# Kernel optimization log

Hardware: AMD Instinct MI355X
Metric: run time of the kernel (lower is better)

## Reference

```python
import jax, jax.numpy as jnp
import numpy as np

K = 16
REP = 128
ASZ = 6
AENC = 64
BSK = 2048 * K  # bs*K flat batch


def _lin(k, fin, fout):
    return jax.random.normal(k, (fin, fout), jnp.float32) / np.float32(np.sqrt(fin))


def setup_inputs() -> dict:
    key = jax.random.key(0)
    ks = jax.random.split(key, 20)
    inp = {
        "lambda1": jax.random.normal(ks[0], (BSK, REP), jnp.float32),
        "actions": jax.random.normal(ks[1], (BSK, ASZ), jnp.float32),
    }
    # (fan_in, hidden, fan_out) per rlkit Mlp((hidden,), out, in)
    specs = {
        "le": (REP, REP, REP),            # lambda_encoder
        "ae": (ASZ, REP, AENC),           # action_encoder
        "aef": (AENC + REP, REP, REP),    # action_effect_network
        "aat": (AENC + REP, REP, 1),      # action_attention_network
        "pe": (2 * REP, 2 * REP, REP),    # pairwise_encoder_network
        "ie": (REP, REP, AENC),           # interaction_effect_network
        "ia": (REP, REP, 1),              # interaction_attention_network
        "fm": (AENC + REP, REP, REP),     # final_merge_network
    }
    i = 2
    for name, (fin, h, fout) in specs.items():
        inp[name + "_W1"] = _lin(ks[i], fin, h)
        inp[name + "_b1"] = jnp.zeros((h,), jnp.float32)
        inp[name + "_W2"] = _lin(ks[i + 1], h, fout)
        inp[name + "_b2"] = jnp.zeros((fout,), jnp.float32)
        i += 2
    return inp


def _mlp(x, W1, b1, W2, b2, out_act):
    h = jax.nn.elu(x @ W1 + b1)
    return out_act(h @ W2 + b2)


# constant all-pairs index lists (i != j), i-major as in the torch loop
_II = np.array([i for i in range(K) for j in range(K) if i != j])
_JJ = np.array([j for i in range(K) for j in range(K) if i != j])


def reference(lambda1, actions,
              le_W1, le_b1, le_W2, le_b2,
              ae_W1, ae_b1, ae_W2, ae_b2,
              aef_W1, aef_b1, aef_W2, aef_b2,
              aat_W1, aat_b1, aat_W2, aat_b2,
              pe_W1, pe_b1, pe_W2, pe_b2,
              ie_W1, ie_b1, ie_W2, ie_b2,
              ia_W1, ia_b1, ia_W2, ia_b2,
              fm_W1, fm_b1, fm_W2, fm_b2):
    elu, sig = jax.nn.elu, jax.nn.sigmoid
    ident = lambda z: z

    enc_flat = _mlp(lambda1, le_W1, le_b1, le_W2, le_b2, elu)        # (BSK, REP)
    a_enc = _mlp(actions, ae_W1, ae_b1, ae_W2, ae_b2, elu)           # (BSK, AENC)
    la = jnp.concatenate([enc_flat, a_enc], -1)                      # (BSK, REP+AENC)
    a_eff = _mlp(la, aef_W1, aef_b1, aef_W2, aef_b2, elu)            # (BSK, REP)
    a_att = _mlp(la, aat_W1, aat_b1, aat_W2, aat_b2, sig)            # (BSK, 1)
    enc = (a_eff * a_att).reshape(-1, K, REP)                        # (bs, K, REP)
    bs = enc.shape[0]

    # all ordered pairs (i, j), i != j -> concat sender/receiver states
    all_pairs = jnp.concatenate([enc[:, _II], enc[:, _JJ]], -1)      # (bs, K*(K-1), 2*REP)
    all_pairs = all_pairs.reshape(bs * K, K - 1, 2 * REP)

    pi = _mlp(all_pairs, pe_W1, pe_b1, pe_W2, pe_b2, elu)            # (bs*K, K-1, REP)
    effect = _mlp(pi, ie_W1, ie_b1, ie_W2, ie_b2, elu)               # (bs*K, K-1, AENC)
    attention = _mlp(pi, ia_W1, ia_b1, ia_W2, ia_b2, sig)            # (bs*K, K-1, 1)
    total_effect = (effect * attention).sum(1)                       # (bs*K, AENC)

    lam_eff = jnp.concatenate([enc_flat, total_effect], -1)          # (bs*K, REP+AENC)
    new_lambdas = _mlp(lam_eff, fm_W1, fm_b1, fm_W2, fm_b2, ident)   # (bs*K, REP)
    return new_lambdas
```

## Files before the change

### kernel.cpp

```cpp
#include <hip/hip_runtime.h>

typedef unsigned short ushort_t;
typedef unsigned int uint_t;
typedef short bf16x8 __attribute__((ext_vector_type(8)));
typedef float f32x4 __attribute__((ext_vector_type(4)));

#define MFMA16(a, b, c) __builtin_amdgcn_mfma_f32_16x16x32_bf16((a), (b), (c), 0, 0, 0)

__device__ __forceinline__ ushort_t f2bf(float f) {
  uint_t u = __float_as_uint(f);
  u += 0x7fffu + ((u >> 16) & 1u);
  return (ushort_t)(u >> 16);
}
__device__ __forceinline__ float bf2f(ushort_t h) {
  return __uint_as_float(((uint_t)h) << 16);
}
__device__ __forceinline__ float eluf(float x) {
  float e = __expf(x) - 1.0f;
  return x > 0.0f ? x : e;
}
__device__ __forceinline__ float sigmf(float x) {
  return 1.0f / (1.0f + __expf(-x));
}

constexpr int BSK = 32768;
constexpr size_t OFF_ENCF = 0;
constexpr size_t OFF_ENC  = 4194304;
constexpr size_t OFF_TEFF = 8388608;
constexpr size_t OFF_FR   = 10485760;

constexpr int FR_LE_W1  = 0;
constexpr int FR_LE_W2  = 16384;
constexpr int FR_AE_W2  = 32768;
constexpr int FR_AEF_W1 = 40960;
constexpr int FR_AAT_W1 = 65536;
constexpr int FR_AEF_W2 = 90112;
constexpr int FR_PE_W1  = 106496;
constexpr int FR_PE_W2  = 172032;
constexpr int FR_IE_W1  = 204800;
constexpr int FR_IE_W2  = 221184;
constexpr int FR_IA_W1  = 229376;
constexpr int FR_FM_W1  = 245760;
constexpr int FR_FM_W2  = 270336;

struct PrepDesc { const float* src; ushort_t* dst; int K; int N; };
struct PrepArgs { PrepDesc d[13]; };

__global__ __launch_bounds__(256) void prep_kernel(PrepArgs a) {
  PrepDesc p = a.d[blockIdx.y];
  int idx = blockIdx.x * 256 + threadIdx.x;
  if (idx >= p.K * p.N) return;
  int e = idx & 7;
  int lane = (idx >> 3) & 63;
  int f = idx >> 9;
  int ksteps = p.K >> 5;
  int kstep = f % ksteps;
  int ntile = f / ksteps;
  int k = kstep * 32 + ((lane >> 4) << 3) + e;
  int n = ntile * 16 + (lane & 15);
  p.dst[idx] = f2bf(p.src[k * p.N + n]);
}


template <int MT, int NT, int KS>
__device__ __forceinline__ void reg_gemm(const bf16x8 a[MT][KS],
                                         const ushort_t* __restrict__ wfrag,
                                         int ntile0, int lane, f32x4 acc[MT][NT]) {
  const f32x4 z = {0.f, 0.f, 0.f, 0.f};
#pragma unroll
  for (int nt = 0; nt < NT; ++nt) {
#pragma unroll
    for (int m = 0; m < MT; ++m) acc[m][nt] = z;
    const ushort_t* wf = wfrag + (size_t)((ntile0 + nt) * KS) * 512 + lane * 8;
#pragma unroll
    for (int ks = 0; ks < KS; ++ks) {
      bf16x8 bfr = *(const bf16x8*)(wf + ks * 512);
#pragma unroll
      for (int m = 0; m < MT; ++m) acc[m][nt] = MFMA16(a[m][ks], bfr, acc[m][nt]);
    }
  }
}

template <int MT, int NT, int KS>
__device__ __forceinline__ void lds_gemm(const ushort_t* __restrict__ Abase,
                                         const ushort_t* __restrict__ wfrag,
                                         int ntile0, int lane, f32x4 acc[MT][NT]) {
  const int r = lane & 15, q = lane >> 4;
  const int swz = (r & 7) << 4;
  bf16x8 a[MT][KS];
#pragma unroll
  for (int m = 0; m < MT; ++m)
#pragma unroll
    for (int ks = 0; ks < KS; ++ks) {
      int row = m * 16 + r;
      int colb = (ks * 64 + q * 16) ^ swz;
      a[m][ks] = *(const bf16x8*)((const char*)Abase + row * (KS * 64) + colb);
    }
  reg_gemm<MT, NT, KS>(a, wfrag, ntile0, lane, acc);
}

template <int MT, int NT, bool ELU>
__device__ __forceinline__ void add_bias_act(f32x4 acc[MT][NT], const float* __restrict__ bias,
                                             int col0, int lane) {
  const int r = lane & 15;
#pragma unroll
  for (int nt = 0; nt < NT; ++nt) {
    float bv = bias[col0 + nt * 16 + r];
#pragma unroll
    for (int m = 0; m < MT; ++m)
#pragma unroll
      for (int k = 0; k < 4; ++k) {
        float v = acc[m][nt][k] + bv;
        acc[m][nt][k] = ELU ? eluf(v) : v;
      }
  }
}

template <int MT, int NT, int CCB>
__device__ __forceinline__ void store_lds(ushort_t* Dbase, int col0, int lane,
                                          const f32x4 acc[MT][NT]) {
  const int cr = lane & 15, cq = lane >> 4;
#pragma unroll
  for (int m = 0; m < MT; ++m)
#pragma unroll
    for (int nt = 0; nt < NT; ++nt)
#pragma unroll
      for (int k = 0; k < 4; ++k) {
        int row = m * 16 + cq * 4 + k;
        int colb = ((col0 + nt * 16 + cr) * 2) ^ ((row & 7) << 4);
        *(ushort_t*)((char*)Dbase + row * CCB + colb) = f2bf(acc[m][nt][k]);
      }
}

template <int MT, int NT>
__device__ __forceinline__ void store_global(ushort_t* __restrict__ G, int row0, int ncols,
                                             int col0, int lane, const f32x4 acc[MT][NT]) {
  const int cr = lane & 15, cq = lane >> 4;
#pragma unroll
  for (int m = 0; m < MT; ++m)
#pragma unroll
    for (int nt = 0; nt < NT; ++nt)
#pragma unroll
      for (int k = 0; k < 4; ++k) {
        int row = m * 16 + cq * 4 + k;
        G[(size_t)(row0 + row) * ncols + col0 + nt * 16 + cr] = f2bf(acc[m][nt][k]);
      }
}

template <int MT, int NT>
__device__ __forceinline__ void store_global_f32(float* __restrict__ G, int row0, int ncols,
                                                 int col0, int lane, const f32x4 acc[MT][NT]) {
  const int cr = lane & 15, cq = lane >> 4;
#pragma unroll
  for (int m = 0; m < MT; ++m)
#pragma unroll
    for (int nt = 0; nt < NT; ++nt)
#pragma unroll
      for (int k = 0; k < 4; ++k) {
        int row = m * 16 + cq * 4 + k;
        G[(size_t)(row0 + row) * ncols + col0 + nt * 16 + cr] = acc[m][nt][k];
      }
}

__global__ __launch_bounds__(256, 2) void enc_kernel(
    const float* __restrict__ lambda1, const float* __restrict__ actions,
    const float* __restrict__ le_b1, const float* __restrict__ le_b2,
    const float* __restrict__ ae_W1, const float* __restrict__ ae_b1,
    const float* __restrict__ ae_b2, const float* __restrict__ aef_b1,
    const float* __restrict__ aef_b2, const float* __restrict__ aat_b1,
    const float* __restrict__ aat_W2, const float* __restrict__ aat_b2,
    const ushort_t* __restrict__ fr, ushort_t* __restrict__ encf, ushort_t* __restrict__ enc) {
  __shared__ ushort_t bufA[64 * 128];
  __shared__ ushort_t bufB[64 * 128];
  __shared__ ushort_t la[64 * 192];
  __shared__ float att[64];

  const int t = threadIdx.x, lane = t & 63, w = t >> 6;
  const int rows0 = blockIdx.x * 64;

  {
    const int row = t >> 2, c0 = (t & 3) * 32;
    const float4* src = (const float4*)(lambda1 + (size_t)(rows0 + row) * 128 + c0);
    const int swz = (row & 7) << 4;
#pragma unroll
    for (int j = 0; j < 8; ++j) {
      float4 v = src[j];
      uint2 p;
      p.x = (uint_t)f2bf(v.x) | ((uint_t)f2bf(v.y) << 16);
      p.y = (uint_t)f2bf(v.z) | ((uint_t)f2bf(v.w) << 16);
      int colb = ((c0 + j * 4) * 2) ^ swz;
      *(uint2*)((char*)bufA + row * 256 + colb) = p;
    }
  }
  __syncthreads();

  f32x4 acc2[4][2];
  lds_gemm<4, 2, 4>(bufA, fr + FR_LE_W1, w * 2, lane, acc2);
  add_bias_act<4, 2, true>(acc2, le_b1, w * 32, lane);
  store_lds<4, 2, 256>(bufB, w * 32, lane, acc2);
  __syncthreads();
  lds_gemm<4, 2, 4>(bufB, fr + FR_LE_W2, w * 2, lane, acc2);
  add_bias_act<4, 2, true>(acc2, le_b2, w * 32, lane);
  store_lds<4, 2, 384>(la, w * 32, lane, acc2);
  store_global<4, 2>(encf, rows0, 128, w * 32, lane, acc2);
  {
    const int row = t >> 2, c0 = (t & 3) * 32;
    float a6[6];
#pragma unroll
    for (int k2 = 0; k2 < 6; ++k2) a6[k2] = actions[(size_t)(rows0 + row) * 6 + k2];
    const int swz = (row & 7) << 4;
#pragma unroll
    for (int j = 0; j < 16; ++j) {
      int c = c0 + j * 2;
      float s0 = ae_b1[c], s1 = ae_b1[c + 1];
#pragma unroll
      for (int k2 = 0; k2 < 6; ++k2) {
        s0 += a6[k2] * ae_W1[k2 * 128 + c];
        s1 += a6[k2] * ae_W1[k2 * 128 + c + 1];
      }
      uint_t pp = (uint_t)f2bf(eluf(s0)) | ((uint_t)f2bf(eluf(s1)) << 16);
      *(uint_t*)((char*)bufA + row * 256 + ((c * 2) ^ swz)) = pp;
    }
  }
  __syncthreads();
  {
    f32x4 acc1[4][1];
    lds_gemm<4, 1, 4>(bufA, fr + FR_AE_W2, w, lane, acc1);
    add_bias_act<4, 1, true>(acc1, ae_b2, w * 16, lane);
    store_lds<4, 1, 384>(la, 128 + w * 16, lane, acc1);
  }
  __syncthreads();
  lds_gemm<4, 2, 6>(la, fr + FR_AEF_W1, w * 2, lane, acc2);
  add_bias_act<4, 2, true>(acc2, aef_b1, w * 32, lane);
  store_lds<4, 2, 256>(bufA, w * 32, lane, acc2);
  lds_gemm<4, 2, 6>(la, fr + FR_AAT_W1, w * 2, lane, acc2);
  add_bias_act<4, 2, true>(acc2, aat_b1, w * 32, lane);
  store_lds<4, 2, 256>(bufB, w * 32, lane, acc2);
  __syncthreads();
  lds_gemm<4, 2, 4>(bufA, fr + FR_AEF_W2, w * 2, lane, acc2);
  add_bias_act<4, 2, true>(acc2, aef_b2, w * 32, lane);
  {
    const int row = t >> 2, s = t & 3;
    const int swz = (row & 7) << 4;
    float sum = 0.f;
#pragma unroll
    for (int j = 0; j < 32; ++j) {
      int c = s * 32 + j;
      sum += bf2f(*(const ushort_t*)((const char*)bufB + row * 256 + ((c * 2) ^ swz))) * aat_W2[c];
    }
    sum += __shfl_xor(sum, 1);
    sum += __shfl_xor(sum, 2);
    if (s == 0) att[row] = sigmf(sum + aat_b2[0]);
  }
  __syncthreads();
  {
    const int cr = lane & 15, cq = lane >> 4;
#pragma unroll
    for (int m = 0; m < 4; ++m)
#pragma unroll
      for (int nt = 0; nt < 2; ++nt)
#pragma unroll
        for (int k = 0; k < 4; ++k) {
          int row = m * 16 + cq * 4 + k;
          enc[(size_t)(rows0 + row) * 128 + w * 32 + nt * 16 + cr] =
              f2bf(acc2[m][nt][k] * att[row]);
        }
  }
}

__global__ __launch_bounds__(256, 3) void pair_kernel(
    const ushort_t* __restrict__ enc, const ushort_t* __restrict__ fr,
    const float* __restrict__ pe_b1, const float* __restrict__ pe_b2,
    const float* __restrict__ ie_b1, const float* __restrict__ ie_b2,
    const float* __restrict__ ia_b1, const float* __restrict__ ia_W2,
    const float* __restrict__ ia_b2, ushort_t* __restrict__ teff) {
  __shared__ ushort_t bufH[32 * 256];
  __shared__ ushort_t bufPi[32 * 128];
  __shared__ float att[32];

  const int t = threadIdx.x, lane = t & 63, w = t >> 6;
  const int r = lane & 15, q = lane >> 4;
  const int g0 = blockIdx.x * 2;
  const int b = g0 >> 4;

  bf16x8 a[2][8];
#pragma unroll
  for (int m = 0; m < 2; ++m) {
    const int im = (g0 + m) & 15;
#pragma unroll
    for (int ks = 0; ks < 8; ++ks) {
      const int srow = (ks < 4) ? im : r;
      const int k = (ks & 3) * 32 + q * 8;
      a[m][ks] = *(const bf16x8*)(enc + (size_t)(b * 16 + srow) * 128 + k);
    }
  }
  {
    f32x4 acc[2][4];
    reg_gemm<2, 4, 8>(a, fr + FR_PE_W1, w * 4, lane, acc);
    add_bias_act<2, 4, true>(acc, pe_b1, w * 64, lane);
    store_lds<2, 4, 512>(bufH, w * 64, lane, acc);
  }
  __syncthreads();
  {
    f32x4 acc[2][2];
    lds_gemm<2, 2, 8>(bufH, fr + FR_PE_W2, w * 2, lane, acc);
    add_bias_act<2, 2, true>(acc, pe_b2, w * 32, lane);
    store_lds<2, 2, 256>(bufPi, w * 32, lane, acc);
  }
  __syncthreads();
  {
    f32x4 acc[2][2];
    lds_gemm<2, 2, 4>(bufPi, fr + FR_IE_W1, w * 2, lane, acc);
    add_bias_act<2, 2, true>(acc, ie_b1, w * 32, lane);
    store_lds<2, 2, 256>(bufH, w * 32, lane, acc);
    lds_gemm<2, 2, 4>(bufPi, fr + FR_IA_W1, w * 2, lane, acc);
    add_bias_act<2, 2, true>(acc, ia_b1, w * 32, lane);
    store_lds<2, 2, 256>(bufH + 32 * 128, w * 32, lane, acc);
  }
  __syncthreads();
  f32x4 eff[2][1];
  lds_gemm<2, 1, 4>(bufH, fr + FR_IE_W2, w, lane, eff);
  add_bias_act<2, 1, true>(eff, ie_b2, w * 16, lane);
  {
    const int row = t >> 3, s = t & 7;
    const int swz = (row & 7) << 4;
    const char* hia = (const char*)(bufH + 32 * 128) + row * 256;
    float sum = 0.f;
#pragma unroll
    for (int j = 0; j < 16; ++j) {
      int c = s * 16 + j;
      sum += bf2f(*(const ushort_t*)(hia + ((c * 2) ^ swz))) * ia_W2[c];
    }
    sum += __shfl_xor(sum, 1);
    sum += __shfl_xor(sum, 2);
    sum += __shfl_xor(sum, 4);
    if (s == 0) att[row] = sigmf(sum + ia_b2[0]);
  }
  __syncthreads();
#pragma unroll
  for (int m = 0; m < 2; ++m) {
    const int im = (g0 + m) & 15;
    float part = 0.f;
#pragma unroll
    for (int k = 0; k < 4; ++k) {
      const int j = q * 4 + k;
      part += (j == im) ? 0.f : eff[m][0][k] * att[m * 16 + j];
    }
    part += __shfl_xor(part, 16);
    part += __shfl_xor(part, 32);
    if (q == 0) teff[(size_t)(g0 + m) * 64 + w * 16 + r] = f2bf(part);
  }
}

__global__ __launch_bounds__(256, 2) void fm_kernel(
    const ushort_t* __restrict__ encf, const ushort_t* __restrict__ teff,
    const ushort_t* __restrict__ fr, const float* __restrict__ fm_b1,
    const float* __restrict__ fm_b2, float* __restrict__ out) {
  __shared__ ushort_t bufH[64 * 128];
  const int t = threadIdx.x, lane = t & 63, w = t >> 6;
  const int rows0 = blockIdx.x * 64;
  const int r = lane & 15, q = lane >> 4;

  bf16x8 a[4][6];
#pragma unroll
  for (int m = 0; m < 4; ++m) {
    const size_t row = rows0 + m * 16 + r;
#pragma unroll
    for (int ks = 0; ks < 6; ++ks) {
      a[m][ks] = (ks < 4) ? *(const bf16x8*)(encf + row * 128 + ks * 32 + q * 8)
                          : *(const bf16x8*)(teff + row * 64 + (ks - 4) * 32 + q * 8);
    }
  }
  f32x4 acc[4][2];
  reg_gemm<4, 2, 6>(a, fr + FR_FM_W1, w * 2, lane, acc);
  add_bias_act<4, 2, true>(acc, fm_b1, w * 32, lane);
  store_lds<4, 2, 256>(bufH, w * 32, lane, acc);
  __syncthreads();
  lds_gemm<4, 2, 4>(bufH, fr + FR_FM_W2, w * 2, lane, acc);
  add_bias_act<4, 2, false>(acc, fm_b2, w * 32, lane);
  store_global_f32<4, 2>(out, rows0, 128, w * 32, lane, acc);
}

extern "C" void kernel_launch(void* const* d_in, const int* in_sizes, int n_in,
                              void* d_out, int out_size, void* d_ws, size_t ws_size,
                              hipStream_t stream) {
  (void)in_sizes; (void)n_in; (void)out_size; (void)ws_size;
  const float* lambda1 = (const float*)d_in[0];
  const float* actions = (const float*)d_in[1];

  ushort_t* ws = (ushort_t*)d_ws;
  ushort_t* encf = ws + OFF_ENCF;
  ushort_t* enc  = ws + OFF_ENC;
  ushort_t* teff = ws + OFF_TEFF;
  ushort_t* fr   = ws + OFF_FR;

  PrepArgs pa;
  const int src_idx[13] = {2, 4, 8, 10, 14, 12, 18, 20, 22, 24, 26, 30, 32};
  const int foff[13] = {FR_LE_W1, FR_LE_W2, FR_AE_W2, FR_AEF_W1, FR_AAT_W1, FR_AEF_W2,
                        FR_PE_W1, FR_PE_W2, FR_IE_W1, FR_IE_W2, FR_IA_W1, FR_FM_W1, FR_FM_W2};
  const int Ks[13] = {128, 128, 128, 192, 192, 128, 256, 256, 128, 128, 128, 192, 128};
  const int Ns[13] = {128, 128, 64, 128, 128, 128, 256, 128, 128, 64, 128, 128, 128};
  for (int i = 0; i < 13; ++i) {
    pa.d[i].src = (const float*)d_in[src_idx[i]];
    pa.d[i].dst = fr + foff[i];
    pa.d[i].K = Ks[i];
    pa.d[i].N = Ns[i];
  }
  prep_kernel<<<dim3(256, 13), 256, 0, stream>>>(pa);

  enc_kernel<<<512, 256, 0, stream>>>(
      lambda1, actions,
      (const float*)d_in[3], (const float*)d_in[5],
      (const float*)d_in[6], (const float*)d_in[7],
      (const float*)d_in[9],
      (const float*)d_in[11], (const float*)d_in[13],
      (const float*)d_in[15], (const float*)d_in[16],
      (const float*)d_in[17],
      fr, encf, enc);

  pair_kernel<<<16384, 256, 0, stream>>>(
      enc, fr,
      (const float*)d_in[19], (const float*)d_in[21],
      (const float*)d_in[23], (const float*)d_in[25],
      (const float*)d_in[27], (const float*)d_in[28],
      (const float*)d_in[29],
      teff);

  fm_kernel<<<512, 256, 0, stream>>>(encf, teff, fr,
                                     (const float*)d_in[31], (const float*)d_in[33],
                                     (float*)d_out);
}
```

Before: 399.9 us.

## Swap MFMA operand order so accumulators are row-contiguous for vectorized stores

Swaps the A/B operands of every MFMA so each lane holds four consecutive output columns of one row. Epilogue stores to LDS and global memory become packed 8-byte bf16 and 16-byte fp32 vector writes instead of scalar 2-byte ones. Bias loads are vectorized accordingly. The attention-weighted sum in the pair kernel is reworked into a 16-lane shuffle reduction. The aim is fewer store instructions and less LDS and global write traffic, in exchange for more shuffles in the reduction.

New measurement: 409.1 us. +2.3%, slower.

```diff
diff --git a/kernel.cpp b/kernel.cpp
--- a/kernel.cpp
+++ b/kernel.cpp
@@ -1,4 +1,5 @@
 #include <hip/hip_runtime.h>
+#include <hip/hip_bf16.h>
 
 typedef unsigned short ushort_t;
 typedef unsigned int uint_t;
@@ -15,6 +16,17 @@
 __device__ __forceinline__ float bf2f(ushort_t h) {
   return __uint_as_float(((uint_t)h) << 16);
 }
+__device__ __forceinline__ uint_t pack2(float lo, float hi) {
+  union { __hip_bfloat162 h; uint_t u; } cv;
+  cv.h = __float22bfloat162_rn(float2{lo, hi});
+  return cv.u;
+}
+__device__ __forceinline__ uint2 pack4(f32x4 v) {
+  uint2 o;
+  o.x = pack2(v[0], v[1]);
+  o.y = pack2(v[2], v[3]);
+  return o;
+}
 __device__ __forceinline__ float eluf(float x) {
   float e = __expf(x) - 1.0f;
   return x > 0.0f ? x : e;
@@ -22,8 +34,10 @@
 __device__ __forceinline__ float sigmf(float x) {
   return 1.0f / (1.0f + __expf(-x));
 }
-
-constexpr int BSK = 32768;
+__device__ __forceinline__ int lds_off(int row, int colb, int ccb) {
+  return row * ccb + (colb ^ ((row & 7) << 4));
+}
+
 constexpr size_t OFF_ENCF = 0;
 constexpr size_t OFF_ENC  = 4194304;
 constexpr size_t OFF_TEFF = 8388608;
@@ -63,9 +77,9 @@
 
 
 template <int MT, int NT, int KS>
-__device__ __forceinline__ void reg_gemm(const bf16x8 a[MT][KS],
-                                         const ushort_t* __restrict__ wfrag,
-                                         int ntile0, int lane, f32x4 acc[MT][NT]) {
+__device__ __forceinline__ void reg_gemm_t(const bf16x8 x[MT][KS],
+                                           const ushort_t* __restrict__ wfrag,
+                                           int ntile0, int lane, f32x4 acc[MT][NT]) {
   const f32x4 z = {0.f, 0.f, 0.f, 0.f};
 #pragma unroll
   for (int nt = 0; nt < NT; ++nt) {
@@ -74,92 +88,71 @@
     const ushort_t* wf = wfrag + (size_t)((ntile0 + nt) * KS) * 512 + lane * 8;
 #pragma unroll
     for (int ks = 0; ks < KS; ++ks) {
-      bf16x8 bfr = *(const bf16x8*)(wf + ks * 512);
-#pragma unroll
-      for (int m = 0; m < MT; ++m) acc[m][nt] = MFMA16(a[m][ks], bfr, acc[m][nt]);
+      bf16x8 wfr = *(const bf16x8*)(wf + ks * 512);
+#pragma unroll
+      for (int m = 0; m < MT; ++m) acc[m][nt] = MFMA16(wfr, x[m][ks], acc[m][nt]);
     }
   }
 }
 
 template <int MT, int NT, int KS>
-__device__ __forceinline__ void lds_gemm(const ushort_t* __restrict__ Abase,
-                                         const ushort_t* __restrict__ wfrag,
-                                         int ntile0, int lane, f32x4 acc[MT][NT]) {
-  const int r = lane & 15, q = lane >> 4;
-  const int swz = (r & 7) << 4;
-  bf16x8 a[MT][KS];
+__device__ __forceinline__ void lds_gemm_t(const ushort_t* __restrict__ Abase,
+                                           const ushort_t* __restrict__ wfrag,
+                                           int ntile0, int lane, f32x4 acc[MT][NT]) {
+  const int r = lane & 15, q = lane >> 4;
+  bf16x8 x[MT][KS];
 #pragma unroll
   for (int m = 0; m < MT; ++m)
 #pragma unroll
     for (int ks = 0; ks < KS; ++ks) {
       int row = m * 16 + r;
-      int colb = (ks * 64 + q * 16) ^ swz;
-      a[m][ks] = *(const bf16x8*)((const char*)Abase + row * (KS * 64) + colb);
-    }
-  reg_gemm<MT, NT, KS>(a, wfrag, ntile0, lane, acc);
+      x[m][ks] = *(const bf16x8*)((const char*)Abase + lds_off(row, ks * 64 + q * 16, KS * 64));
+    }
+  reg_gemm_t<MT, NT, KS>(x, wfrag, ntile0, lane, acc);
 }
 
 template <int MT, int NT, bool ELU>
-__device__ __forceinline__ void add_bias_act(f32x4 acc[MT][NT], const float* __restrict__ bias,
-                                             int col0, int lane) {
-  const int r = lane & 15;
+__device__ __forceinline__ void add_bias_act_t(f32x4 acc[MT][NT], const float* __restrict__ bias,
+                                               int col0, int lane) {
+  const int q = lane >> 4;
 #pragma unroll
   for (int nt = 0; nt < NT; ++nt) {
-    float bv = bias[col0 + nt * 16 + r];
+    f32x4 bv = *(const f32x4*)(bias + col0 + nt * 16 + q * 4);
 #pragma unroll
     for (int m = 0; m < MT; ++m)
 #pragma unroll
       for (int k = 0; k < 4; ++k) {
-        float v = acc[m][nt][k] + bv;
+        float v = acc[m][nt][k] + bv[k];
         acc[m][nt][k] = ELU ? eluf(v) : v;
       }
   }
 }
 
 template <int MT, int NT, int CCB>
-__device__ __forceinline__ void store_lds(ushort_t* Dbase, int col0, int lane,
-                                          const f32x4 acc[MT][NT]) {
-  const int cr = lane & 15, cq = lane >> 4;
+__device__ __forceinline__ void store_lds_t(ushort_t* Dbase, int col0, int lane,
+                                            const f32x4 acc[MT][NT]) {
+  const int r = lane & 15, q = lane >> 4;
+#pragma unroll
+  for (int m = 0; m < MT; ++m) {
+    const int row = m * 16 + r;
+#pragma unroll
+    for (int nt = 0; nt < NT; ++nt) {
+      int colb = (col0 + nt * 16 + q * 4) * 2;
+      *(uint2*)((char*)Dbase + lds_off(row, colb, CCB)) = pack4(acc[m][nt]);
+    }
+  }
+}
+
+template <int MT, int NT>
+__device__ __forceinline__ void store_global_t(ushort_t* __restrict__ G, int row0, int ncols,
+                                               int col0, int lane, const f32x4 acc[MT][NT]) {
+  const int r = lane & 15, q = lane >> 4;
 #pragma unroll
   for (int m = 0; m < MT; ++m)
 #pragma unroll
     for (int nt = 0; nt < NT; ++nt)
-#pragma unroll
-      for (int k = 0; k < 4; ++k) {
-        int row = m * 16 + cq * 4 + k;
-        int colb = ((col0 + nt * 16 + cr) * 2) ^ ((row & 7) << 4);
-        *(ushort_t*)((char*)Dbase + row * CCB + colb) = f2bf(acc[m][nt][k]);
-      }
-}
-
-template <int MT, int NT>
-__device__ __forceinline__ void store_global(ushort_t* __restrict__ G, int row0, int ncols,
-                                             int col0, int lane, const f32x4 acc[MT][NT]) {
-  const int cr = lane & 15, cq = lane >> 4;
-#pragma unroll
-  for (int m = 0; m < MT; ++m)
-#pragma unroll
-    for (int nt = 0; nt < NT; ++nt)
-#pragma unroll
-      for (int k = 0; k < 4; ++k) {
-        int row = m * 16 + cq * 4 + k;
-        G[(size_t)(row0 + row) * ncols + col0 + nt * 16 + cr] = f2bf(acc[m][nt][k]);
-      }
-}
-
-template <int MT, int NT>
-__device__ __forceinline__ void store_global_f32(float* __restrict__ G, int row0, int ncols,
-                                                 int col0, int lane, const f32x4 acc[MT][NT]) {
-  const int cr = lane & 15, cq = lane >> 4;
-#pragma unroll
-  for (int m = 0; m < MT; ++m)
-#pragma unroll
-    for (int nt = 0; nt < NT; ++nt)
-#pragma unroll
-      for (int k = 0; k < 4; ++k) {
-        int row = m * 16 + cq * 4 + k;
-        G[(size_t)(row0 + row) * ncols + col0 + nt * 16 + cr] = acc[m][nt][k];
-      }
+      *(uint2*)(G + (size_t)(row0 + m * 16 + r) * ncols + col0 + nt * 16 + q * 4) =
+          pack4(acc[m][nt]);
 }
 
 __global__ __launch_bounds__(256, 2) void enc_kernel(
@@ -176,39 +169,35 @@
   __shared__ float att[64];
 
   const int t = threadIdx.x, lane = t & 63, w = t >> 6;
+  const int r = lane & 15, q = lane >> 4;
   const int rows0 = blockIdx.x * 64;
 
   {
     const int row = t >> 2, c0 = (t & 3) * 32;
     const float4* src = (const float4*)(lambda1 + (size_t)(rows0 + row) * 128 + c0);
-    const int swz = (row & 7) << 4;
 #pragma unroll
     for (int j = 0; j < 8; ++j) {
       float4 v = src[j];
-      uint2 p;
-      p.x = (uint_t)f2bf(v.x) | ((uint_t)f2bf(v.y) << 16);
-      p.y = (uint_t)f2bf(v.z) | ((uint_t)f2bf(v.w) << 16);
-      int colb = ((c0 + j * 4) * 2) ^ swz;
-      *(uint2*)((char*)bufA + row * 256 + colb) = p;
+      f32x4 vv = {v.x, v.y, v.z, v.w};
+      *(uint2*)((char*)bufA + lds_off(row, (c0 + j * 4) * 2, 256)) = pack4(vv);
     }
   }
   __syncthreads();
 
   f32x4 acc2[4][2];
-  lds_gemm<4, 2, 4>(bufA, fr + FR_LE_W1, w * 2, lane, acc2);
-  add_bias_act<4, 2, true>(acc2, le_b1, w * 32, lane);
-  store_lds<4, 2, 256>(bufB, w * 32, lane, acc2);
-  __syncthreads();
-  lds_gemm<4, 2, 4>(bufB, fr + FR_LE_W2, w * 2, lane, acc2);
-  add_bias_act<4, 2, true>(acc2, le_b2, w * 32, lane);
-  store_lds<4, 2, 384>(la, w * 32, lane, acc2);
-  store_global<4, 2>(encf, rows0, 128, w * 32, lane, acc2);
+  lds_gemm_t<4, 2, 4>(bufA, fr + FR_LE_W1, w * 2, lane, acc2);
+  add_bias_act_t<4, 2, true>(acc2, le_b1, w * 32, lane);
+  store_lds_t<4, 2, 256>(bufB, w * 32, lane, acc2);
+  __syncthreads();
+  lds_gemm_t<4, 2, 4>(bufB, fr + FR_LE_W2, w * 2, lane, acc2);
+  add_bias_act_t<4, 2, true>(acc2, le_b2, w * 32, lane);
+  store_lds_t<4, 2, 384>(la, w * 32, lane, acc2);
+  store_global_t<4, 2>(encf, rows0, 128, w * 32, lane, acc2);
   {
     const int row = t >> 2, c0 = (t & 3) * 32;
     float a6[6];
 #pragma unroll
     for (int k2 = 0; k2 < 6; ++k2) a6[k2] = actions[(size_t)(rows0 + row) * 6 + k2];
-    const int swz = (row & 7) << 4;
 #pragma unroll
     for (int j = 0; j < 16; ++j) {
       int c = c0 + j * 2;
@@ -218,53 +207,48 @@
         s0 += a6[k2] * ae_W1[k2 * 128 + c];
         s1 += a6[k2] * ae_W1[k2 * 128 + c + 1];
       }
-      uint_t pp = (uint_t)f2bf(eluf(s0)) | ((uint_t)f2bf(eluf(s1)) << 16);
-      *(uint_t*)((char*)bufA + row * 256 + ((c * 2) ^ swz)) = pp;
+      *(uint_t*)((char*)bufA + lds_off(row, c * 2, 256)) = pack2(eluf(s0), eluf(s1));
     }
   }
   __syncthreads();
   {
     f32x4 acc1[4][1];
-    lds_gemm<4, 1, 4>(bufA, fr + FR_AE_W2, w, lane, acc1);
-    add_bias_act<4, 1, true>(acc1, ae_b2, w * 16, lane);
-    store_lds<4, 1, 384>(la, 128 + w * 16, lane, acc1);
-  }
-  __syncthreads();
-  lds_gemm<4, 2, 6>(la, fr + FR_AEF_W1, w * 2, lane, acc2);
-  add_bias_act<4, 2, true>(acc2, aef_b1, w * 32, lane);
-  store_lds<4, 2, 256>(bufA, w * 32, lane, acc2);
-  lds_gemm<4, 2, 6>(la, fr + FR_AAT_W1, w * 2, lane, acc2);
-  add_bias_act<4, 2, true>(acc2, aat_b1, w * 32, lane);
-  store_lds<4, 2, 256>(bufB, w * 32, lane, acc2);
-  __syncthreads();
-  lds_gemm<4, 2, 4>(bufA, fr + FR_AEF_W2, w * 2, lane, acc2);
-  add_bias_act<4, 2, true>(acc2, aef_b2, w * 32, lane);
+    lds_gemm_t<4, 1, 4>(bufA, fr + FR_AE_W2, w, lane, acc1);
+    add_bias_act_t<4, 1, true>(acc1, ae_b2, w * 16, lane);
+    store_lds_t<4, 1, 384>(la, 128 + w * 16, lane, acc1);
+  }
+  __syncthreads();
+  lds_gemm_t<4, 2, 6>(la, fr + FR_AEF_W1, w * 2, lane, acc2);
+  add_bias_act_t<4, 2, true>(acc2, aef_b1, w * 32, lane);
+  store_lds_t<4, 2, 256>(bufA, w * 32, lane, acc2);
+  lds_gemm_t<4, 2, 6>(la, fr + FR_AAT_W1, w * 2, lane, acc2);
+  add_bias_act_t<4, 2, true>(acc2, aat_b1, w * 32, lane);
+  store_lds_t<4, 2, 256>(bufB, w * 32, lane, acc2);
+  __syncthreads();
+  lds_gemm_t<4, 2, 4>(bufA, fr + FR_AEF_W2, w * 2, lane, acc2);
+  add_bias_act_t<4, 2, true>(acc2, aef_b2, w * 32, lane);
   {
     const int row = t >> 2, s = t & 3;
-    const int swz = (row & 7) << 4;
     float sum = 0.f;
 #pragma unroll
     for (int j = 0; j < 32; ++j) {
       int c = s * 32 + j;
-      sum += bf2f(*(const ushort_t*)((const char*)bufB + row * 256 + ((c * 2) ^ swz))) * aat_W2[c];
+      sum += bf2f(*(const ushort_t*)((const char*)bufB + lds_off(row, c * 2, 256))) * aat_W2[c];
     }
     sum += __shfl_xor(sum, 1);
     sum += __shfl_xor(sum, 2);
     if (s == 0) att[row] = sigmf(sum + aat_b2[0]);
   }
   __syncthreads();
-  {
-    const int cr = lane & 15, cq = lane >> 4;
-#pragma unroll
-    for (int m = 0; m < 4; ++m)
-#pragma unroll
-      for (int nt = 0; nt < 2; ++nt)
-#pragma unroll
-        for (int k = 0; k < 4; ++k) {
-          int row = m * 16 + cq * 4 + k;
-          enc[(size_t)(rows0 + row) * 128 + w * 32 + nt * 16 + cr] =
-              f2bf(acc2[m][nt][k] * att[row]);
-        }
+#pragma unroll
+  for (int mt = 0; mt < 4; ++mt) {
+    float av = att[mt * 16 + r];
+#pragma unroll
+    for (int nt = 0; nt < 2; ++nt) {
+      f32x4 sv = acc2[mt][nt];
+      sv[0] *= av; sv[1] *= av; sv[2] *= av; sv[3] *= av;
+      *(uint2*)(enc + (size_t)(rows0 + mt * 16 + r) * 128 + w * 32 + nt * 16 + q * 4) = pack4(sv);
+    }
   }
 }
 
@@ -283,53 +267,52 @@
   const int g0 = blockIdx.x * 2;
   const int b = g0 >> 4;
 
-  bf16x8 a[2][8];
-#pragma unroll
-  for (int m = 0; m < 2; ++m) {
-    const int im = (g0 + m) & 15;
+  bf16x8 x[2][8];
+#pragma unroll
+  for (int mt = 0; mt < 2; ++mt) {
+    const int im = (g0 + mt) & 15;
 #pragma unroll
     for (int ks = 0; ks < 8; ++ks) {
       const int srow = (ks < 4) ? im : r;
       const int k = (ks & 3) * 32 + q * 8;
-      a[m][ks] = *(const bf16x8*)(enc + (size_t)(b * 16 + srow) * 128 + k);
+      x[mt][ks] = *(const bf16x8*)(enc + (size_t)(b * 16 + srow) * 128 + k);
     }
   }
   {
     f32x4 acc[2][4];
-    reg_gemm<2, 4, 8>(a, fr + FR_PE_W1, w * 4, lane, acc);
-    add_bias_act<2, 4, true>(acc, pe_b1, w * 64, lane);
-    store_lds<2, 4, 512>(bufH, w * 64, lane, acc);
+    reg_gemm_t<2, 4, 8>(x, fr + FR_PE_W1, w * 4, lane, acc);
+    add_bias_act_t<2, 4, true>(acc, pe_b1, w * 64, lane);
+    store_lds_t<2, 4, 512>(bufH, w * 64, lane, acc);
   }
   __syncthreads();
   {
     f32x4 acc[2][2];
-    lds_gemm<2, 2, 8>(bufH, fr + FR_PE_W2, w * 2, lane, acc);
-    add_bias_act<2, 2, true>(acc, pe_b2, w * 32, lane);
-    store_lds<2, 2, 256>(bufPi, w * 32, lane, acc);
+    lds_gemm_t<2, 2, 8>(bufH, fr + FR_PE_W2, w * 2, lane, acc);
+    add_bias_act_t<2, 2, true>(acc, pe_b2, w * 32, lane);
+    store_lds_t<2, 2, 256>(bufPi, w * 32, lane, acc);
   }
   __syncthreads();
   {
     f32x4 acc[2][2];
-    lds_gemm<2, 2, 4>(bufPi, fr + FR_IE_W1, w * 2, lane, acc);
-    add_bias_act<2, 2, true>(acc, ie_b1, w * 32, lane);
-    store_lds<2, 2, 256>(bufH, w * 32, lane, acc);
-    lds_gemm<2, 2, 4>(bufPi, fr + FR_IA_W1, w * 2, lane, acc);
-    add_bias_act<2, 2, true>(acc, ia_b1, w * 32, lane);
-    store_lds<2, 2, 256>(bufH + 32 * 128, w * 32, lane, acc);
+    lds_gemm_t<2, 2, 4>(bufPi, fr + FR_IE_W1, w * 2, lane, acc);
+    add_bias_act_t<2, 2, true>(acc, ie_b1, w * 32, lane);
+    store_lds_t<2, 2, 256>(bufH, w * 32, lane, acc);
+    lds_gemm_t<2, 2, 4>(bufPi, fr + FR_IA_W1, w * 2, lane, acc);
+    add_bias_act_t<2, 2, true>(acc, ia_b1, w * 32, lane);
+    store_lds_t<2, 2, 256>(bufH + 32 * 128, w * 32, lane, acc);
   }
   __syncthreads();
   f32x4 eff[2][1];
-  lds_gemm<2, 1, 4>(bufH, fr + FR_IE_W2, w, lane, eff);
-  add_bias_act<2, 1, true>(eff, ie_b2, w * 16, lane);
+  lds_gemm_t<2, 1, 4>(bufH, fr + FR_IE_W2, w, lane, eff);
+  add_bias_act_t<2, 1, true>(eff, ie_b2, w * 16, lane);
   {
     const int row = t >> 3, s = t & 7;
-    const int swz = (row & 7) << 4;
-    const char* hia = (const char*)(bufH + 32 * 128) + row * 256;
+    const char* hia = (const char*)(bufH + 32 * 128);
     float sum = 0.f;
 #pragma unroll
     for (int j = 0; j < 16; ++j) {
       int c = s * 16 + j;
-      sum += bf2f(*(const ushort_t*)(hia + ((c * 2) ^ swz))) * ia_W2[c];
+      sum += bf2f(*(const ushort_t*)(hia + lds_off(row, c * 2, 256))) * ia_W2[c];
     }
     sum += __shfl_xor(sum, 1);
     sum += __shfl_xor(sum, 2);
@@ -338,17 +321,24 @@
   }
   __syncthreads();
 #pragma unroll
-  for (int m = 0; m < 2; ++m) {
-    const int im = (g0 + m) & 15;
-    float part = 0.f;
-#pragma unroll
-    for (int k = 0; k < 4; ++k) {
-      const int j = q * 4 + k;
-      part += (j == im) ? 0.f : eff[m][0][k] * att[m * 16 + j];
-    }
-    part += __shfl_xor(part, 16);
-    part += __shfl_xor(part, 32);
-    if (q == 0) teff[(size_t)(g0 + m) * 64 + w * 16 + r] = f2bf(part);
+  for (int mt = 0; mt < 2; ++mt) {
+    const int im = (g0 + mt) & 15;
+    const float av = (r == im) ? 0.f : att[mt * 16 + r];
+    float v0 = eff[mt][0][0] * av, v1 = eff[mt][0][1] * av;
+    float v2 = eff[mt][0][2] * av, v3 = eff[mt][0][3] * av;
+#pragma unroll
+    for (int d = 1; d < 16; d <<= 1) {
+      v0 += __shfl_xor(v0, d);
+      v1 += __shfl_xor(v1, d);
+      v2 += __shfl_xor(v2, d);
+      v3 += __shfl_xor(v3, d);
+    }
+    if (r == 0) {
+      uint2 p;
+      p.x = pack2(v0, v1);
+      p.y = pack2(v2, v3);
+      *(uint2*)(teff + (size_t)(g0 + mt) * 64 + w * 16 + q * 4) = p;
+    }
   }
 }
 
@@ -358,27 +348,32 @@
     const float* __restrict__ fm_b2, float* __restrict__ out) {
   __shared__ ushort_t bufH[64 * 128];
   const int t = threadIdx.x, lane = t & 63, w = t >> 6;
+  const int r = lane & 15, q = lane >> 4;
   const int rows0 = blockIdx.x * 64;
-  const int r = lane & 15, q = lane >> 4;
-
-  bf16x8 a[4][6];
-#pragma unroll
-  for (int m = 0; m < 4; ++m) {
-    const size_t row = rows0 + m * 16 + r;
+
+  bf16x8 x[4][6];
+#pragma unroll
+  for (int mt = 0; mt < 4; ++mt) {
+    const size_t row = rows0 + mt * 16 + r;
 #pragma unroll
     for (int ks = 0; ks < 6; ++ks) {
-      a[m][ks] = (ks < 4) ? *(const bf16x8*)(encf + row * 128 + ks * 32 + q * 8)
-                          : *(const bf16x8*)(teff + row * 64 + (ks - 4) * 32 + q * 8);
+      x[mt][ks] = (ks < 4) ? *(const bf16x8*)(encf + row * 128 + ks * 32 + q * 8)
+                           : *(const bf16x8*)(teff + row * 64 + (ks - 4) * 32 + q * 8);
     }
   }
   f32x4 acc[4][2];
-  reg_gemm<4, 2, 6>(a, fr + FR_FM_W1, w * 2, lane, acc);
-  add_bias_act<4, 2, true>(acc, fm_b1, w * 32, lane);
-  store_lds<4, 2, 256>(bufH, w * 32, lane, acc);
-  __syncthreads();
-  lds_gemm<4, 2, 4>(bufH, fr + FR_FM_W2, w * 2, lane, acc);
-  add_bias_act<4, 2, false>(acc, fm_b2, w * 32, lane);
-  store_global_f32<4, 2>(out, rows0, 128, w * 32, lane, acc);
+  reg_gemm_t<4, 2, 6>(x, fr + FR_FM_W1, w * 2, lane, acc);
+  add_bias_act_t<4, 2, true>(acc, fm_b1, w * 32, lane);
+  store_lds_t<4, 2, 256>(bufH, w * 32, lane, acc);
+  __syncthreads();
+  lds_gemm_t<4, 2, 4>(bufH, fr + FR_FM_W2, w * 2, lane, acc);
+  add_bias_act_t<4, 2, false>(acc, fm_b2, w * 32, lane);
+#pragma unroll
+  for (int mt = 0; mt < 4; ++mt)
+#pragma unroll
+    for (int nt = 0; nt < 2; ++nt)
+      *(f32x4*)(out + (size_t)(rows0 + mt * 16 + r) * 128 + w * 32 + nt * 16 + q * 4) =
+          acc[mt][nt];
 }
 
 extern "C" void kernel_launch(void* const* d_in, const int* in_sizes, int n_in,
```
